# Performance work log

Measured on AMD Instinct MI355X. Metric: run time of the kernel, lower is better.

Reference implementation:

```python
import jax, jax.numpy as jnp
import numpy as np

B, Q, N0, N1, N2 = 2, 16, 4096, 1024, 256
DIM, CTX, HEADS = 296, 288, 8
I1, I2, I3 = 144, 72, 36
EPS = 1e-5  # BatchNorm eps (eval mode)


def setup_inputs():
    key = jax.random.key(0)
    ks = iter(jax.random.split(key, 64))
    def rn(shape, scale=1.0):
        return scale * jax.random.normal(next(ks), shape, dtype=jnp.float32)
    def ru(shape, lo, hi):
        return jax.random.uniform(next(ks), shape, dtype=jnp.float32, minval=lo, maxval=hi)
    def bn(c):  # rows: gamma, beta, running_mean, running_var
        return jnp.stack([1.0 + 0.1 * rn((c,)), 0.1 * rn((c,)), 0.1 * rn((c,)), 1.0 + 0.1 * jnp.abs(rn((c,)))])
    def lin(o, i):
        s = 1.0 / np.sqrt(i)
        return rn((o, i), s), rn((o,), s)
    w1, b1 = lin(DIM, DIM); w2, b2 = lin(I1, DIM)
    a1_w, a1_b = lin(I2, 3); a2_w, a2_b = lin(I1, 128)
    fp1_w1, fp1_b1 = lin(I1, 2 * I1); fp1_w2, fp1_b2 = lin(I2, I1)
    fp2_w1, fp2_b1 = lin(I2, 2 * I2); fp2_w2, fp2_b2 = lin(I3, I2)
    out_w, out_b = lin(1, I3)
    return {
        "x": rn((B, CTX, N2)),
        "bbox_mask": ru((B, Q, HEADS, N2), 0.0, 1.0),
        "sa0_features": rn((B, 3, N0)),
        "sa1_features": rn((B, 128, N1)),
        "sa0_xyz": ru((B, N0, 3), -1.0, 1.0),
        "sa1_xyz": ru((B, N1, 3), -1.0, 1.0),
        "sa2_xyz": ru((B, N2, 3), -1.0, 1.0),
        "w1": w1, "b1": b1, "bn1": bn(DIM),
        "w2": w2, "b2": b2, "bn2": bn(I1),
        "a1_w": a1_w, "a1_b": a1_b,
        "a2_w": a2_w, "a2_b": a2_b,
        "fp1_w1": fp1_w1, "fp1_b1": fp1_b1, "fp1_bn1": bn(I1),
        "fp1_w2": fp1_w2, "fp1_b2": fp1_b2, "fp1_bn2": bn(I2),
        "fp2_w1": fp2_w1, "fp2_b1": fp2_b1, "fp2_bn1": bn(I2),
        "fp2_w2": fp2_w2, "fp2_b2": fp2_b2, "fp2_bn2": bn(I3),
        "out_w": out_w, "out_b": out_b,
    }


def _expand(t, q):
    # tensor.unsqueeze(1).repeat(1, q, 1, 1).flatten(0, 1)
    b = t.shape[0]
    return jnp.broadcast_to(t[:, None], (b, q) + t.shape[1:]).reshape((b * q,) + t.shape[1:])


def _bn(x, p):
    g, b, m, v = p  # (C,) each; x: (BQ, C, N)
    return (x - m[:, None]) * (g * jax.lax.rsqrt(v + EPS))[:, None] + b[:, None]


def _layer(x, W, b, p):
    # SharedMLP layer: 1x1 Conv2d + BN(eval) + ReLU on (BQ, C, N[, 1])
    return jax.nn.relu(_bn(jnp.einsum('oc,bcn->bon', W, x) + b[None, :, None], p))


def _three_interpolate(unknown_xyz, known_xyz, known_feats):
    # three_nn: squared dists (BQ, Nu, Nk) -> 3 smallest; inverse-distance weights
    d2 = jnp.sum((unknown_xyz[:, :, None, :] - known_xyz[:, None, :, :]) ** 2, axis=-1)
    neg_d, idx = jax.lax.top_k(-d2, 3)
    w = 1.0 / (-neg_d + 1e-8)
    w = w / jnp.sum(w, axis=-1, keepdims=True)  # (BQ, Nu, 3)
    g = jax.vmap(lambda f, i: f[:, i])(known_feats, idx)  # (BQ, C, Nu, 3)
    return jnp.sum(g * w[:, None], axis=-1)  # (BQ, C, Nu)


def reference(x, bbox_mask, sa0_features, sa1_features, sa0_xyz, sa1_xyz, sa2_xyz, w1, b1, bn1, w2, b2, bn2, a1_w, a1_b, a2_w, a2_b, fp1_w1, fp1_b1, fp1_bn1, fp1_w2, fp1_b2, fp1_bn2, fp2_w1, fp2_b1, fp2_bn1, fp2_w2, fp2_b2, fp2_bn2, out_w, out_b):
    q = bbox_mask.shape[1]
    h = jnp.concatenate([_expand(x, q), bbox_mask.reshape((-1,) + bbox_mask.shape[2:])], axis=1)  # (BQ, DIM, N2)
    h = _layer(h, w1, b1, bn1)
    h = _layer(h, w2, b2, bn2)  # (BQ, I1, N2)
    f0 = jnp.einsum('oc,bcn->bon', a1_w, sa0_features) + a1_b[None, :, None]  # adapter1
    f1 = jnp.einsum('oc,bcn->bon', a2_w, sa1_features) + a2_b[None, :, None]  # adapter2
    f0, f1 = _expand(f0, q), _expand(f1, q)
    xyz0, xyz1, xyz2 = _expand(sa0_xyz, q), _expand(sa1_xyz, q), _expand(sa2_xyz, q)
    # FP1: propagate sa2 -> sa1, concat [interpolated, skip] as in PointnetFPModule
    h = jnp.concatenate([_three_interpolate(xyz1, xyz2, h), f1], axis=1)
    h = _layer(h, fp1_w1, fp1_b1, fp1_bn1)
    h = _layer(h, fp1_w2, fp1_b2, fp1_bn2)
    # FP2: propagate sa1 -> sa0
    h = jnp.concatenate([_three_interpolate(xyz0, xyz1, h), f0], axis=1)
    h = _layer(h, fp2_w1, fp2_b1, fp2_bn1)
    h = _layer(h, fp2_w2, fp2_b2, fp2_bn2)  # (BQ, I3, N0)
    out = jnp.einsum('oc,bcn->bon', out_w, h) + out_b[None, :, None]  # (BQ, 1, N0)
    return out
```

## Files before the change

### kernel.cpp

```cpp
#include <hip/hip_runtime.h>

#define EPS_BN 1e-5f
typedef float v2f __attribute__((ext_vector_type(2)));

struct LayerDesc {
    const float* W; const float* b; const float* bn;
    float* wt; float* shb; int O; int C;
};
struct HeadArgs {
    LayerDesc l[6];
    const float* a2w; const float* a2b; const float* w3; const float* b3; const float* bn3;
    float* w3c; float* sh3;
    const float* a1w; const float* a1b; const float* w5; const float* b5; const float* bn5;
    float* w5c; float* sh5;
    const float* xyz0; const float* xyz1; const float* xyz2;
    int* idx1; float* wgt1; int* idx2; float* wgt2;
};

__global__ __launch_bounds__(256) void head_kernel(HeadArgs a) {
    const int bx = blockIdx.x, tid = threadIdx.x;
    if (bx < 96) {
        LayerDesc d = a.l[bx / 16];
        int sub = bx % 16;
        int total = d.O * d.C;
        for (int i = sub * 256 + tid; i < total; i += 16 * 256) {
            int c = i / d.O, o = i - (i / d.O) * d.O;
            float sc = 1.f;
            if (d.bn) { float g = d.bn[o], v = d.bn[3 * d.O + o]; sc = g * rsqrtf(v + EPS_BN); }
            d.wt[i] = d.W[(size_t)o * d.C + c] * sc;
        }
        for (int o = sub * 256 + tid; o < d.O; o += 16 * 256) {
            float sc = 1.f, sh = 0.f;
            if (d.bn) {
                float g = d.bn[o], be = d.bn[d.O + o], m = d.bn[2 * d.O + o], v = d.bn[3 * d.O + o];
                sc = g * rsqrtf(v + EPS_BN); sh = be - m * sc;
            }
            d.shb[o] = d.b[o] * sc + sh;
        }
        return;
    } else if (bx < 169) {
        int e = (bx - 96) * 256 + tid;
        if (e < 128 * 144) {
            int k = e / 144, o = e - (e / 144) * 144;
            float sc = a.bn3[o] * rsqrtf(a.bn3[3 * 144 + o] + EPS_BN);
            float s = 0.f;
            for (int c = 0; c < 144; ++c)
                s += a.a2w[c * 128 + k] * a.w3[(size_t)o * 288 + 144 + c];
            a.w3c[k * 144 + o] = s * sc;
        } else if (e < 128 * 144 + 144) {
            int o = e - 128 * 144;
            float g = a.bn3[o], be = a.bn3[144 + o], m = a.bn3[2 * 144 + o], v = a.bn3[3 * 144 + o];
            float sc = g * rsqrtf(v + EPS_BN);
            float s = 0.f;
            for (int c = 0; c < 144; ++c) s += a.w3[(size_t)o * 288 + 144 + c] * a.a2b[c];
            a.sh3[o] = (s + a.b3[o] - m) * sc + be;
        }
        return;
    } else if (bx < 171) {
        int e = (bx - 169) * 256 + tid;
        if (e < 3 * 72) {
            int k = e / 72, o = e - (e / 72) * 72;
            float sc = a.bn5[o] * rsqrtf(a.bn5[3 * 72 + o] + EPS_BN);
            float s = 0.f;
            for (int c = 0; c < 72; ++c)
                s += a.a1w[c * 3 + k] * a.w5[(size_t)o * 144 + 72 + c];
            a.w5c[k * 72 + o] = s * sc;
        } else if (e < 3 * 72 + 72) {
            int o = e - 3 * 72;
            float g = a.bn5[o], be = a.bn5[72 + o], m = a.bn5[2 * 72 + o], v = a.bn5[3 * 72 + o];
            float sc = g * rsqrtf(v + EPS_BN);
            float s = 0.f;
            for (int c = 0; c < 72; ++c) s += a.w5[(size_t)o * 144 + 72 + c] * a.a1b[c];
            a.sh5[o] = (s + a.b5[o] - m) * sc + be;
        }
        return;
    }
    const int NSEG = 8;
    __shared__ float kl[3 * 1024];
    __shared__ float sd[NSEG][32][3];
    __shared__ int   si[NSEG][32][3];
    const float* unknown; const float* known;
    int Nu, Nk, blk, b; int* idx; float* wgt;
    int t = bx - 171;
    if (t < 64) {
        unknown = a.xyz1; known = a.xyz2; Nu = 1024; Nk = 256;
        b = t >> 5; blk = t & 31; idx = a.idx1; wgt = a.wgt1;
    } else {
        t -= 64;
        unknown = a.xyz0; known = a.xyz1; Nu = 4096; Nk = 1024;
        b = t >> 7; blk = t & 127; idx = a.idx2; wgt = a.wgt2;
    }
    for (int i = tid; i < Nk * 3; i += 256) kl[i] = known[(size_t)b * Nk * 3 + i];
    __syncthreads();
    const int u   = tid & 31;
    const int seg = tid >> 5;
    const int n   = blk * 32 + u;
    const float* up = unknown + ((size_t)b * Nu + n) * 3;
    const float ux = up[0], uy = up[1], uz = up[2];
    float d0 = 1e30f, d1 = 1e30f, d2 = 1e30f;
    int i0 = 0, i1 = 0, i2 = 0;
    const int klo = seg * (Nk / NSEG), khi = klo + Nk / NSEG;
    for (int k = klo; k < khi; ++k) {
        float dx = __fsub_rn(ux, kl[3 * k + 0]);
        float dy = __fsub_rn(uy, kl[3 * k + 1]);
        float dz = __fsub_rn(uz, kl[3 * k + 2]);
        float d = __fadd_rn(__fadd_rn(__fmul_rn(dx, dx), __fmul_rn(dy, dy)), __fmul_rn(dz, dz));
        if (d < d0)      { d2 = d1; i2 = i1; d1 = d0; i1 = i0; d0 = d; i0 = k; }
        else if (d < d1) { d2 = d1; i2 = i1; d1 = d;  i1 = k; }
        else if (d < d2) { d2 = d;  i2 = k; }
    }
    sd[seg][u][0] = d0; sd[seg][u][1] = d1; sd[seg][u][2] = d2;
    si[seg][u][0] = i0; si[seg][u][1] = i1; si[seg][u][2] = i2;
    __syncthreads();
    if (tid < 32) {
        float m0 = 1e30f, m1 = 1e30f, m2 = 1e30f;
        int j0 = 0, j1 = 0, j2 = 0;
        for (int s = 0; s < NSEG; ++s)
            for (int c = 0; c < 3; ++c) {
                float d = sd[s][u][c];
                int ii = si[s][u][c];
                if (d < m0)      { m2 = m1; j2 = j1; m1 = m0; j1 = j0; m0 = d; j0 = ii; }
                else if (d < m1) { m2 = m1; j2 = j1; m1 = d;  j1 = ii; }
                else if (d < m2) { m2 = d;  j2 = ii; }
            }
        float w0 = 1.f / (m0 + 1e-8f), w1 = 1.f / (m1 + 1e-8f), w2 = 1.f / (m2 + 1e-8f);
        float s = w0 + w1 + w2;
        size_t base = ((size_t)b * Nu + n) * 3;
        idx[base + 0] = j0; idx[base + 1] = j1; idx[base + 2] = j2;
        wgt[base + 0] = w0 / s; wgt[base + 1] = w1 / s; wgt[base + 2] = w2 / s;
    }
}

template <int BLK, int CT, int O, int OT, bool RELU, int ADD, bool TOUT>
__device__ __forceinline__ void conv_body(
    int nt, int ot, int nb, int tid,
    const float* __restrict__ src0, int qdiv0,
    const float* __restrict__ Wt, const float* __restrict__ shb,
    const float* __restrict__ basep, int qdivb,
    float* __restrict__ outp, int N, float* wlds)
{
    static_assert(OT % 4 == 0, "OT float4 grouping");
    static_assert(CT % 8 == 0 || CT % 8 == 4, "CT pipeline tail");
    const int oBase = ot * OT;
    const int n0 = (nt * BLK + tid) * 4;

    for (int i = tid; i < CT * OT; i += BLK)
        wlds[i] = Wt[(size_t)(i / OT) * O + oBase + (i % OT)];
    __syncthreads();

    const float* s0 = src0 + (size_t)(nb / qdiv0) * CT * N + n0;

    v2f acc[OT][2];
#pragma unroll
    for (int ol = 0; ol < OT; ++ol) { acc[ol][0] = (v2f)0.f; acc[ol][1] = (v2f)0.f; }

    auto loadrow = [&](float (&x)[4], int c) {
        float4 t = *reinterpret_cast<const float4*>(s0 + (size_t)c * N);
        x[0] = t.x; x[1] = t.y; x[2] = t.z; x[3] = t.w;
    };
    auto comprow = [&](const float (&x)[4], int c) {
        v2f x01; x01[0] = x[0]; x01[1] = x[1];
        v2f x23; x23[0] = x[2]; x23[1] = x[3];
#pragma unroll
        for (int g = 0; g < OT / 4; ++g) {
            float4 wv = *reinterpret_cast<const float4*>(&wlds[c * OT + g * 4]);
            float ww[4] = {wv.x, wv.y, wv.z, wv.w};
#pragma unroll
            for (int r = 0; r < 4; ++r) {
                v2f w2; w2[0] = ww[r]; w2[1] = ww[r];
                acc[g * 4 + r][0] = __builtin_elementwise_fma(w2, x01, acc[g * 4 + r][0]);
                acc[g * 4 + r][1] = __builtin_elementwise_fma(w2, x23, acc[g * 4 + r][1]);
            }
        }
    };
    auto loadg = [&](float (&buf)[4][4], int c) {
#pragma unroll
        for (int q = 0; q < 4; ++q) loadrow(buf[q], c + q);
    };
    auto compg = [&](const float (&buf)[4][4], int c) {
#pragma unroll
        for (int q = 0; q < 4; ++q) comprow(buf[q], c + q);
    };

    {
        float xa[4][4], xb[4][4];
        loadg(xa, 0); loadg(xb, 4);
        int c = 0;
#pragma unroll 1
        for (; c + 16 <= CT; c += 8) {
            compg(xa, c);     loadg(xa, c + 8);
            compg(xb, c + 4); loadg(xb, c + 12);
        }
        compg(xa, c);
        if constexpr (CT % 8 == 4) {
            loadg(xa, c + 8);
            compg(xb, c + 4);
            compg(xa, c + 8);
        } else {
            compg(xb, c + 4);
        }
    }

    if constexpr (TOUT) {
#pragma unroll
        for (int j = 0; j < 4; ++j) {
            float4 t;
            t.x = acc[0][j >> 1][j & 1];
            t.y = acc[1][j >> 1][j & 1];
            t.z = acc[2][j >> 1][j & 1];
            t.w = acc[3][j >> 1][j & 1];
            *reinterpret_cast<float4*>(outp + ((size_t)nb * N + n0 + j) * O + oBase) = t;
        }
        return;
    }

    const float* bp = (ADD == 2) ? (basep + ((size_t)(nb / qdivb) * O + oBase) * N + n0) : nullptr;
#pragma unroll
    for (int ol = 0; ol < OT; ++ol) {
        int o = oBase + ol;
        float addv[4];
        if constexpr (ADD == 2) {
            float4 t = *reinterpret_cast<const float4*>(bp + (size_t)ol * N);
            addv[0] = t.x; addv[1] = t.y; addv[2] = t.z; addv[3] = t.w;
        } else if constexpr (ADD == 1) {
            float sb = shb[o];
#pragma unroll
            for (int j = 0; j < 4; ++j) addv[j] = sb;
        } else {
#pragma unroll
            for (int j = 0; j < 4; ++j) addv[j] = 0.f;
        }
        float res[4];
#pragma unroll
        for (int j = 0; j < 4; ++j) {
            float y = acc[ol][j >> 1][j & 1] + addv[j];
            if constexpr (RELU) y = fmaxf(y, 0.f);
            res[j] = y;
        }
        float4 t; t.x = res[0]; t.y = res[1]; t.z = res[2]; t.w = res[3];
        *reinterpret_cast<float4*>(outp + ((size_t)nb * O + o) * N + n0) = t;
    }
}

template <int BLK, int CT, int O, int OT, bool RELU, int ADD, bool TOUT>
__global__ __launch_bounds__(BLK) void conv_swz(
    const float* __restrict__ src0, int qdiv0,
    const float* __restrict__ Wt, const float* __restrict__ shb,
    const float* __restrict__ basep, int qdivb,
    float* __restrict__ outp, int N, int GX, int GY)
{
    __shared__ __align__(16) float wlds[CT * OT];
    int f = blockIdx.x;
    int J = gridDim.x >> 3;
    int j = (f & 7) * J + (f >> 3);
    int ot = j % GY; int r = j / GY;
    int nt = r % GX; int nb = r / GX;
    conv_body<BLK, CT, O, OT, RELU, ADD, TOUT>(
        nt, ot, nb, threadIdx.x, src0, qdiv0, Wt, shb, basep, qdivb, outp, N, wlds);
}

__global__ __launch_bounds__(64) void bases_kernel(
    const float* __restrict__ x, const float* __restrict__ sa1f,
    const float* __restrict__ wt1, const float* __restrict__ sb1,
    const float* __restrict__ w3c, const float* __restrict__ sh3,
    float* __restrict__ base1, float* __restrict__ base3)
{
    __shared__ __align__(16) float wlds[288 * 4];
    const int bx = blockIdx.x, tid = threadIdx.x;
    if (bx < 148) {
        int ot = bx % 74, nb = bx / 74;
        conv_body<64, 288, 296, 4, false, 1, false>(0, ot, nb, tid, x, 1, wt1, sb1, nullptr, 1, base1, 256, wlds);
    } else {
        int lb = bx - 148;
        int nt = lb % 4, ot = (lb / 4) % 36, nb = lb / 144;
        conv_body<64, 128, 144, 4, false, 1, false>(nt, ot, nb, tid, sa1f, 1, w3c, sh3, nullptr, 1, base3, 1024, wlds);
    }
}

__global__ __launch_bounds__(64) void gather_t1_kernel(
    const float* __restrict__ g3t,
    const int* __restrict__ idx, const float* __restrict__ wgt,
    const float* __restrict__ base3,
    float* __restrict__ h3)
{
    int f = blockIdx.x;
    int j = (f & 7) * 64 + (f >> 3);
    int nb = j >> 4, nt = j & 15;
    int lane = threadIdx.x;
    int n = nt * 64 + lane;
    int b = nb >> 4;
    size_t nn = ((size_t)b * 1024 + n) * 3;
    int j0 = idx[nn], j1 = idx[nn + 1], j2 = idx[nn + 2];
    float w0 = wgt[nn], w1 = wgt[nn + 1], w2 = wgt[nn + 2];
    const float* gbase = g3t + (size_t)nb * 256 * 144;
    const float* p0 = gbase + (size_t)j0 * 144;
    const float* p1 = gbase + (size_t)j1 * 144;
    const float* p2 = gbase + (size_t)j2 * 144;
    const float* bb = base3 + (size_t)b * 144 * 1024 + n;
    float* ob = h3 + (size_t)nb * 144 * 1024 + n;
#pragma unroll 1
    for (int cc = 0; cc < 144; cc += 8) {
        float4 a0 = *reinterpret_cast<const float4*>(p0 + cc);
        float4 a0b = *reinterpret_cast<const float4*>(p0 + cc + 4);
        float4 a1 = *reinterpret_cast<const float4*>(p1 + cc);
        float4 a1b = *reinterpret_cast<const float4*>(p1 + cc + 4);
        float4 a2 = *reinterpret_cast<const float4*>(p2 + cc);
        float4 a2b = *reinterpret_cast<const float4*>(p2 + cc + 4);
        float r0[8] = {a0.x, a0.y, a0.z, a0.w, a0b.x, a0b.y, a0b.z, a0b.w};
        float r1[8] = {a1.x, a1.y, a1.z, a1.w, a1b.x, a1b.y, a1b.z, a1b.w};
        float r2[8] = {a2.x, a2.y, a2.z, a2.w, a2b.x, a2b.y, a2b.z, a2b.w};
#pragma unroll
        for (int r = 0; r < 8; ++r) {
            float v = w0 * r0[r] + w1 * r1[r] + w2 * r2[r] + bb[(size_t)(cc + r) * 1024];
            ob[(size_t)(cc + r) * 1024] = fmaxf(v, 0.f);
        }
    }
}

__global__ __launch_bounds__(64) void h6out_kernel(
    const float* __restrict__ g5t,
    const int* __restrict__ idx, const float* __restrict__ wgt,
    const float* __restrict__ sa0,
    const float* __restrict__ w5c, const float* __restrict__ sh5,
    const float* __restrict__ Wt6, const float* __restrict__ shb6,
    const float* __restrict__ wout, const float* __restrict__ bout,
    float* __restrict__ outp)
{
    __shared__ __align__(16) float wlds[72 * 36];
    __shared__ float w5l[3 * 72];
    __shared__ float sh5l[72], ow[36], sh6l[36];
    const int tid = threadIdx.x;
    for (int i = tid; i < 72 * 36; i += 64) wlds[i] = Wt6[i];
    for (int i = tid; i < 216; i += 64) w5l[i] = w5c[i];
    for (int i = tid; i < 72; i += 64) sh5l[i] = sh5[i];
    if (tid < 36) { ow[tid] = wout[tid]; sh6l[tid] = shb6[tid]; }
    __syncthreads();
    int f = blockIdx.x;
    int j = (f & 7) * ((int)gridDim.x >> 3) + (f >> 3);
    const int nb = j >> 6;
    const int nt = j & 63;
    const int n = nt * 64 + tid;
    const int b = nb >> 4;
    size_t nn = ((size_t)b * 4096 + n) * 3;
    const int j0 = idx[nn], j1 = idx[nn + 1], j2 = idx[nn + 2];
    const float w0 = wgt[nn], w1 = wgt[nn + 1], w2 = wgt[nn + 2];
    const float* gbase = g5t + (size_t)nb * 1024 * 72;
    const float* p0 = gbase + (size_t)j0 * 72;
    const float* p1 = gbase + (size_t)j1 * 72;
    const float* p2 = gbase + (size_t)j2 * 72;
    const float* s0 = sa0 + (size_t)b * 3 * 4096 + n;
    const float sx = s0[0], sy = s0[4096], sz = s0[8192];

    v2f acc[18];
#pragma unroll
    for (int o = 0; o < 18; ++o) acc[o] = (v2f)0.f;

    float ra[8][3], rb[8][3];
    auto ld = [&](float (&r)[8][3], int c) {
        float4 a0 = *reinterpret_cast<const float4*>(p0 + c);
        float4 a0b = *reinterpret_cast<const float4*>(p0 + c + 4);
        float4 a1 = *reinterpret_cast<const float4*>(p1 + c);
        float4 a1b = *reinterpret_cast<const float4*>(p1 + c + 4);
        float4 a2 = *reinterpret_cast<const float4*>(p2 + c);
        float4 a2b = *reinterpret_cast<const float4*>(p2 + c + 4);
        r[0][0] = a0.x; r[1][0] = a0.y; r[2][0] = a0.z; r[3][0] = a0.w;
        r[4][0] = a0b.x; r[5][0] = a0b.y; r[6][0] = a0b.z; r[7][0] = a0b.w;
        r[0][1] = a1.x; r[1][1] = a1.y; r[2][1] = a1.z; r[3][1] = a1.w;
        r[4][1] = a1b.x; r[5][1] = a1b.y; r[6][1] = a1b.z; r[7][1] = a1b.w;
        r[0][2] = a2.x; r[1][2] = a2.y; r[2][2] = a2.z; r[3][2] = a2.w;
        r[4][2] = a2b.x; r[5][2] = a2b.y; r[6][2] = a2b.z; r[7][2] = a2b.w;
    };
    auto cp = [&](const float (&r)[8][3], int c) {
#pragma unroll
        for (int q = 0; q < 8; ++q) {
            int cc = c + q;
            float base = w5l[cc] * sx + w5l[72 + cc] * sy + w5l[144 + cc] * sz + sh5l[cc];
            float xv = fmaxf(w0 * r[q][0] + w1 * r[q][1] + w2 * r[q][2] + base, 0.f);
            v2f xv2; xv2[0] = xv; xv2[1] = xv;
#pragma unroll
            for (int g = 0; g < 9; ++g) {
                float4 wv = *reinterpret_cast<const float4*>(&wlds[cc * 36 + g * 4]);
                v2f wa; wa[0] = wv.x; wa[1] = wv.y;
                v2f wb; wb[0] = wv.z; wb[1] = wv.w;
                acc[g * 2 + 0] = __builtin_elementwise_fma(wa, xv2, acc[g * 2 + 0]);
                acc[g * 2 + 1] = __builtin_elementwise_fma(wb, xv2, acc[g * 2 + 1]);
            }
        }
    };
    ld(ra, 0); ld(rb, 8);
    int c = 0;
#pragma unroll 1
    for (; c + 32 <= 72; c += 16) {
        cp(ra, c);     ld(ra, c + 16);
        cp(rb, c + 8); ld(rb, c + 24);
    }
    cp(ra, 48); ld(ra, 64);
    cp(rb, 56);
    cp(ra, 64);

    float r = bout[0];
#pragma unroll
    for (int o = 0; o < 36; ++o) r += ow[o] * fmaxf(acc[o >> 1][o & 1] + sh6l[o], 0.f);
    outp[(size_t)nb * 4096 + n] = r;
}

extern "C" void kernel_launch(void* const* d_in, const int* in_sizes, int n_in,
                              void* d_out, int out_size, void* d_ws, size_t ws_size,
                              hipStream_t stream) {
    const int B = 2, Q = 16, N0 = 4096, N1 = 1024, N2 = 256;
    const int I1 = 144;
    const int NB = B * Q;

    const float* x     = (const float*)d_in[0];
    const float* mask  = (const float*)d_in[1];
    const float* sa0f  = (const float*)d_in[2];
    const float* sa1f  = (const float*)d_in[3];
    const float* xyz0  = (const float*)d_in[4];
    const float* xyz1  = (const float*)d_in[5];
    const float* xyz2  = (const float*)d_in[6];

    float* ws = (float*)d_ws;
    size_t off = 0;
    auto alloc = [&](size_t n) { size_t p = off; off += (n + 15) & ~(size_t)15; return p; };

    size_t wgt1  = alloc((size_t)B * N1 * 3);
    size_t wgt2  = alloc((size_t)B * N0 * 3);
    size_t idx1  = alloc((size_t)B * N1 * 3);
    size_t idx2  = alloc((size_t)B * N0 * 3);
    size_t slotA = alloc((size_t)NB * 296 * N2);
    size_t slotB = alloc((size_t)NB * I1 * N1);
    size_t base1 = alloc((size_t)B * 296 * N2);
    size_t base3 = alloc((size_t)B * I1 * N1);
    size_t wt1 = alloc(296 * 296), sb1 = alloc(296);
    size_t wt2 = alloc(296 * 144), sb2 = alloc(144);
    size_t wt3 = alloc(288 * 144), sb3 = alloc(144);
    size_t wt4 = alloc(144 * 72),  sb4 = alloc(72);
    size_t wt5 = alloc(144 * 72),  sb5 = alloc(72);
    size_t wt6 = alloc(72 * 36),   sb6 = alloc(36);
    size_t w3c = alloc(128 * 144), sh3 = alloc(144);
    size_t w5c = alloc(3 * 72),    sh5 = alloc(72);
    (void)ws_size; (void)in_sizes; (void)n_in;

    auto din = [&](int i) { return (const float*)d_in[i]; };

    HeadArgs ha;
    ha.l[0] = { din(7),  din(8),  din(9),  ws + wt1, ws + sb1, 296, 296 };
    ha.l[1] = { din(10), din(11), din(12), ws + wt2, ws + sb2, 144, 296 };
    ha.l[2] = { din(17), din(18), din(19), ws + wt3, ws + sb3, 144, 288 };
    ha.l[3] = { din(20), din(21), din(22), ws + wt4, ws + sb4, 72, 144 };
    ha.l[4] = { din(23), din(24), din(25), ws + wt5, ws + sb5, 72, 144 };
    ha.l[5] = { din(26), din(27), din(28), ws + wt6, ws + sb6, 36, 72 };
    ha.a2w = din(15); ha.a2b = din(16); ha.w3 = din(17); ha.b3 = din(18); ha.bn3 = din(19);
    ha.w3c = ws + w3c; ha.sh3 = ws + sh3;
    ha.a1w = din(13); ha.a1b = din(14); ha.w5 = din(23); ha.b5 = din(24); ha.bn5 = din(25);
    ha.w5c = ws + w5c; ha.sh5 = ws + sh5;
    ha.xyz0 = xyz0; ha.xyz1 = xyz1; ha.xyz2 = xyz2;
    ha.idx1 = (int*)(ws + idx1); ha.wgt1 = ws + wgt1;
    ha.idx2 = (int*)(ws + idx2); ha.wgt2 = ws + wgt2;
    head_kernel<<<dim3(171 + 64 + 256), 256, 0, stream>>>(ha);

    bases_kernel<<<dim3(436), 64, 0, stream>>>(
        x, sa1f, ws + wt1, ws + sb1, ws + w3c, ws + sh3, ws + base1, ws + base3);

    conv_swz<64, 8, 296, 4, true, 2, false><<<dim3(2368), 64, 0, stream>>>(
        mask, 1, ws + wt1 + 288 * 296, ws + sb1, ws + base1, Q, ws + slotA, N2, 1, 74);

    conv_swz<64, 296, 144, 4, true, 1, false><<<dim3(1152), 64, 0, stream>>>(
        ws + slotA, 1, ws + wt2, ws + sb2, nullptr, 1, ws + slotB, N2, 1, 36);

    conv_swz<64, 144, 144, 4, false, 0, true><<<dim3(1152), 64, 0, stream>>>(
        ws + slotB, 1, ws + wt3, ws + sb3, nullptr, 1, ws + slotA, N2, 1, 36);

    gather_t1_kernel<<<dim3(512), 64, 0, stream>>>(
        ws + slotA, (const int*)(ws + idx1), ws + wgt1, ws + base3, ws + slotB);

    conv_swz<64, 144, 72, 4, true, 1, false><<<dim3(2304), 64, 0, stream>>>(
        ws + slotB, 1, ws + wt4, ws + sb4, nullptr, 1, ws + slotA, N1, 4, 18);

    conv_swz<64, 72, 72, 4, false, 0, true><<<dim3(2304), 64, 0, stream>>>(
        ws + slotA, 1, ws + wt5, ws + sb5, nullptr, 1, ws + slotB, N1, 4, 18);

    h6out_kernel<<<dim3(2048), 64, 0, stream>>>(
        ws + slotB, (const int*)(ws + idx2), ws + wgt2, sa0f,
        ws + w5c, ws + sh5, ws + wt6, ws + sb6, din(29), din(30), (float*)d_out);
}
```

Measured before the change: 174.4 us.

## Split conv reduction across two waves per block and halve gather channel work

The channel (K) loop of the pointwise conv layers is split between two wavefronts in a 128-thread block, and the partial sums are combined through shared memory. This doubles the number of waves in flight for these small-N layers. The gather kernel now splits its 144 channels into two 72-channel halves, using twice as many blocks. The tiny CT=8 mask conv gets a simpler fully unrolled single-wave kernel. The cost is an extra LDS reduction and barrier per block, and only one wave does the epilogue.

```diff
diff --git a/kernel.cpp b/kernel.cpp
--- a/kernel.cpp
+++ b/kernel.cpp
@@ -131,29 +131,11 @@
     }
 }
 
-template <int BLK, int CT, int O, int OT, bool RELU, int ADD, bool TOUT>
-__device__ __forceinline__ void conv_body(
-    int nt, int ot, int nb, int tid,
-    const float* __restrict__ src0, int qdiv0,
-    const float* __restrict__ Wt, const float* __restrict__ shb,
-    const float* __restrict__ basep, int qdivb,
-    float* __restrict__ outp, int N, float* wlds)
-{
-    static_assert(OT % 4 == 0, "OT float4 grouping");
-    static_assert(CT % 8 == 0 || CT % 8 == 4, "CT pipeline tail");
-    const int oBase = ot * OT;
-    const int n0 = (nt * BLK + tid) * 4;
-
-    for (int i = tid; i < CT * OT; i += BLK)
-        wlds[i] = Wt[(size_t)(i / OT) * O + oBase + (i % OT)];
-    __syncthreads();
-
-    const float* s0 = src0 + (size_t)(nb / qdiv0) * CT * N + n0;
-
-    v2f acc[OT][2];
-#pragma unroll
-    for (int ol = 0; ol < OT; ++ol) { acc[ol][0] = (v2f)0.f; acc[ol][1] = (v2f)0.f; }
-
+template <int CTW>
+__device__ __forceinline__ void conv_kloop(
+    const float* __restrict__ s0, int N, const float* wldsw, v2f (&acc)[4][2])
+{
+    static_assert(CTW % 8 == 0 || CTW % 8 == 4, "CT tail");
     auto loadrow = [&](float (&x)[4], int c) {
         float4 t = *reinterpret_cast<const float4*>(s0 + (size_t)c * N);
         x[0] = t.x; x[1] = t.y; x[2] = t.z; x[3] = t.w;
@@ -161,16 +143,13 @@
     auto comprow = [&](const float (&x)[4], int c) {
         v2f x01; x01[0] = x[0]; x01[1] = x[1];
         v2f x23; x23[0] = x[2]; x23[1] = x[3];
-#pragma unroll
-        for (int g = 0; g < OT / 4; ++g) {
-            float4 wv = *reinterpret_cast<const float4*>(&wlds[c * OT + g * 4]);
-            float ww[4] = {wv.x, wv.y, wv.z, wv.w};
-#pragma unroll
-            for (int r = 0; r < 4; ++r) {
-                v2f w2; w2[0] = ww[r]; w2[1] = ww[r];
-                acc[g * 4 + r][0] = __builtin_elementwise_fma(w2, x01, acc[g * 4 + r][0]);
-                acc[g * 4 + r][1] = __builtin_elementwise_fma(w2, x23, acc[g * 4 + r][1]);
-            }
+        float4 wv = *reinterpret_cast<const float4*>(wldsw + c * 4);
+        float ww[4] = {wv.x, wv.y, wv.z, wv.w};
+#pragma unroll
+        for (int r = 0; r < 4; ++r) {
+            v2f w2; w2[0] = ww[r]; w2[1] = ww[r];
+            acc[r][0] = __builtin_elementwise_fma(w2, x01, acc[r][0]);
+            acc[r][1] = __builtin_elementwise_fma(w2, x23, acc[r][1]);
         }
     };
     auto loadg = [&](float (&buf)[4][4], int c) {
@@ -181,25 +160,61 @@
 #pragma unroll
         for (int q = 0; q < 4; ++q) comprow(buf[q], c + q);
     };
-
-    {
-        float xa[4][4], xb[4][4];
-        loadg(xa, 0); loadg(xb, 4);
-        int c = 0;
+    float xa[4][4], xb[4][4];
+    loadg(xa, 0); loadg(xb, 4);
+    int c = 0;
 #pragma unroll 1
-        for (; c + 16 <= CT; c += 8) {
-            compg(xa, c);     loadg(xa, c + 8);
-            compg(xb, c + 4); loadg(xb, c + 12);
-        }
-        compg(xa, c);
-        if constexpr (CT % 8 == 4) {
-            loadg(xa, c + 8);
-            compg(xb, c + 4);
-            compg(xa, c + 8);
-        } else {
-            compg(xb, c + 4);
-        }
-    }
+    for (; c + 16 <= CTW; c += 8) {
+        compg(xa, c);     loadg(xa, c + 8);
+        compg(xb, c + 4); loadg(xb, c + 12);
+    }
+    compg(xa, c);
+    if constexpr (CTW % 8 == 4) {
+        loadg(xa, c + 8);
+        compg(xb, c + 4);
+        compg(xa, c + 8);
+    } else {
+        compg(xb, c + 4);
+    }
+}
+
+template <int CT0, int CT1, int O, bool RELU, int ADD, bool TOUT>
+__device__ __forceinline__ void conv2w(
+    int nt, int ot, int nb, int tid,
+    const float* __restrict__ src0, int qdiv0,
+    const float* __restrict__ Wt, const float* __restrict__ shb,
+    const float* __restrict__ basep, int qdivb,
+    float* __restrict__ outp, int N, float* wlds, float* sred)
+{
+    constexpr int CTALL = CT0 + CT1;
+    const int wid = tid >> 6, lane = tid & 63;
+    const int oBase = ot * 4;
+    const int n0 = (nt * 64 + lane) * 4;
+
+    for (int i = tid; i < CTALL * 4; i += 128)
+        wlds[i] = Wt[(size_t)(i >> 2) * O + oBase + (i & 3)];
+    __syncthreads();
+
+    const int c0 = wid ? CT0 : 0;
+    const float* s0 = src0 + (size_t)(nb / qdiv0) * CTALL * N + (size_t)c0 * N + n0;
+
+    v2f acc[4][2];
+#pragma unroll
+    for (int r = 0; r < 4; ++r) { acc[r][0] = (v2f)0.f; acc[r][1] = (v2f)0.f; }
+
+    if (wid == 0) conv_kloop<CT0>(s0, N, wlds, acc);
+    else          conv_kloop<CT1>(s0, N, wlds + CT0 * 4, acc);
+
+    if (wid == 1) {
+#pragma unroll
+        for (int i = 0; i < 16; ++i)
+            sred[i * 64 + lane] = acc[i >> 2][(i >> 1) & 1][i & 1];
+    }
+    __syncthreads();
+    if (wid != 0) return;
+#pragma unroll
+    for (int i = 0; i < 16; ++i)
+        acc[i >> 2][(i >> 1) & 1][i & 1] += sred[i * 64 + lane];
 
     if constexpr (TOUT) {
 #pragma unroll
@@ -213,7 +228,92 @@
         }
         return;
     }
-
+    const float* bp = (ADD == 2) ? (basep + ((size_t)(nb / qdivb) * O + oBase) * N + n0) : nullptr;
+#pragma unroll
+    for (int ol = 0; ol < 4; ++ol) {
+        int o = oBase + ol;
+        float addv[4];
+        if constexpr (ADD == 2) {
+            float4 t = *reinterpret_cast<const float4*>(bp + (size_t)ol * N);
+            addv[0] = t.x; addv[1] = t.y; addv[2] = t.z; addv[3] = t.w;
+        } else if constexpr (ADD == 1) {
+            float sb = shb[o];
+#pragma unroll
+            for (int j = 0; j < 4; ++j) addv[j] = sb;
+        } else {
+#pragma unroll
+            for (int j = 0; j < 4; ++j) addv[j] = 0.f;
+        }
+        float res[4];
+#pragma unroll
+        for (int j = 0; j < 4; ++j) {
+            float y = acc[ol][j >> 1][j & 1] + addv[j];
+            if constexpr (RELU) y = fmaxf(y, 0.f);
+            res[j] = y;
+        }
+        float4 t; t.x = res[0]; t.y = res[1]; t.z = res[2]; t.w = res[3];
+        *reinterpret_cast<float4*>(outp + ((size_t)nb * O + o) * N + n0) = t;
+    }
+}
+
+template <int CT0, int CT1, int O, bool RELU, int ADD, bool TOUT>
+__global__ __launch_bounds__(128) void conv_ks2(
+    const float* __restrict__ src0, int qdiv0,
+    const float* __restrict__ Wt, const float* __restrict__ shb,
+    const float* __restrict__ basep, int qdivb,
+    float* __restrict__ outp, int N, int GX, int GY)
+{
+    __shared__ __align__(16) float wlds[(CT0 + CT1) * 4];
+    __shared__ float sred[16 * 64];
+    int f = blockIdx.x;
+    int J = gridDim.x >> 3;
+    int j = (f & 7) * J + (f >> 3);
+    int ot = j % GY; int r = j / GY;
+    int nt = r % GX; int nb = r / GX;
+    conv2w<CT0, CT1, O, RELU, ADD, TOUT>(
+        nt, ot, nb, threadIdx.x, src0, qdiv0, Wt, shb, basep, qdivb, outp, N, wlds, sred);
+}
+
+template <int CT, int O, int OT, bool RELU, int ADD>
+__global__ __launch_bounds__(64) void conv_swz(
+    const float* __restrict__ src0, int qdiv0,
+    const float* __restrict__ Wt, const float* __restrict__ shb,
+    const float* __restrict__ basep, int qdivb,
+    float* __restrict__ outp, int N, int GX, int GY)
+{
+    __shared__ __align__(16) float wlds[CT * OT];
+    int f = blockIdx.x;
+    int J = gridDim.x >> 3;
+    int j = (f & 7) * J + (f >> 3);
+    int ot = j % GY; int r = j / GY;
+    int nt = r % GX; int nb = r / GX;
+    const int lane = threadIdx.x;
+    const int oBase = ot * OT;
+    const int n0 = (nt * 64 + lane) * 4;
+    for (int i = lane; i < CT * OT; i += 64)
+        wlds[i] = Wt[(size_t)(i / OT) * O + oBase + (i % OT)];
+    __builtin_amdgcn_wave_barrier();
+    const float* s0 = src0 + (size_t)(nb / qdiv0) * CT * N + n0;
+    v2f acc[OT][2];
+#pragma unroll
+    for (int ol = 0; ol < OT; ++ol) { acc[ol][0] = (v2f)0.f; acc[ol][1] = (v2f)0.f; }
+#pragma unroll
+    for (int c = 0; c < CT; ++c) {
+        float4 t = *reinterpret_cast<const float4*>(s0 + (size_t)c * N);
+        v2f x01; x01[0] = t.x; x01[1] = t.y;
+        v2f x23; x23[0] = t.z; x23[1] = t.w;
+#pragma unroll
+        for (int g = 0; g < OT / 4; ++g) {
+            float4 wv = *reinterpret_cast<const float4*>(&wlds[c * OT + g * 4]);
+            float ww[4] = {wv.x, wv.y, wv.z, wv.w};
+#pragma unroll
+            for (int r = 0; r < 4; ++r) {
+                v2f w2; w2[0] = ww[r]; w2[1] = ww[r];
+                acc[g * 4 + r][0] = __builtin_elementwise_fma(w2, x01, acc[g * 4 + r][0]);
+                acc[g * 4 + r][1] = __builtin_elementwise_fma(w2, x23, acc[g * 4 + r][1]);
+            }
+        }
+    }
     const float* bp = (ADD == 2) ? (basep + ((size_t)(nb / qdivb) * O + oBase) * N + n0) : nullptr;
 #pragma unroll
     for (int ol = 0; ol < OT; ++ol) {
@@ -242,38 +342,22 @@
     }
 }
 
-template <int BLK, int CT, int O, int OT, bool RELU, int ADD, bool TOUT>
-__global__ __launch_bounds__(BLK) void conv_swz(
-    const float* __restrict__ src0, int qdiv0,
-    const float* __restrict__ Wt, const float* __restrict__ shb,
-    const float* __restrict__ basep, int qdivb,
-    float* __restrict__ outp, int N, int GX, int GY)
-{
-    __shared__ __align__(16) float wlds[CT * OT];
-    int f = blockIdx.x;
-    int J = gridDim.x >> 3;
-    int j = (f & 7) * J + (f >> 3);
-    int ot = j % GY; int r = j / GY;
-    int nt = r % GX; int nb = r / GX;
-    conv_body<BLK, CT, O, OT, RELU, ADD, TOUT>(
-        nt, ot, nb, threadIdx.x, src0, qdiv0, Wt, shb, basep, qdivb, outp, N, wlds);
-}
-
-__global__ __launch_bounds__(64) void bases_kernel(
+__global__ __launch_bounds__(128) void bases_kernel(
     const float* __restrict__ x, const float* __restrict__ sa1f,
     const float* __restrict__ wt1, const float* __restrict__ sb1,
     const float* __restrict__ w3c, const float* __restrict__ sh3,
     float* __restrict__ base1, float* __restrict__ base3)
 {
     __shared__ __align__(16) float wlds[288 * 4];
+    __shared__ float sred[16 * 64];
     const int bx = blockIdx.x, tid = threadIdx.x;
     if (bx < 148) {
         int ot = bx % 74, nb = bx / 74;
-        conv_body<64, 288, 296, 4, false, 1, false>(0, ot, nb, tid, x, 1, wt1, sb1, nullptr, 1, base1, 256, wlds);
+        conv2w<144, 144, 296, false, 1, false>(0, ot, nb, tid, x, 1, wt1, sb1, nullptr, 1, base1, 256, wlds, sred);
     } else {
         int lb = bx - 148;
         int nt = lb % 4, ot = (lb / 4) % 36, nb = lb / 144;
-        conv_body<64, 128, 144, 4, false, 1, false>(nt, ot, nb, tid, sa1f, 1, w3c, sh3, nullptr, 1, base3, 1024, wlds);
+        conv2w<64, 64, 144, false, 1, false>(nt, ot, nb, tid, sa1f, 1, w3c, sh3, nullptr, 1, base3, 1024, wlds, sred);
     }
 }
 
@@ -284,8 +368,9 @@
     float* __restrict__ h3)
 {
     int f = blockIdx.x;
-    int j = (f & 7) * 64 + (f >> 3);
-    int nb = j >> 4, nt = j & 15;
+    int j = (f & 7) * 128 + (f >> 3);
+    int cseg = j & 1; int rest = j >> 1;
+    int nb = rest >> 4, nt = rest & 15;
     int lane = threadIdx.x;
     int n = nt * 64 + lane;
     int b = nb >> 4;
@@ -298,8 +383,9 @@
     const float* p2 = gbase + (size_t)j2 * 144;
     const float* bb = base3 + (size_t)b * 144 * 1024 + n;
     float* ob = h3 + (size_t)nb * 144 * 1024 + n;
+    const int cs = cseg * 72;
 #pragma unroll 1
-    for (int cc = 0; cc < 144; cc += 8) {
+    for (int cc = cs; cc < cs + 72; cc += 8) {
         float4 a0 = *reinterpret_cast<const float4*>(p0 + cc);
         float4 a0b = *reinterpret_cast<const float4*>(p0 + cc + 4);
         float4 a1 = *reinterpret_cast<const float4*>(p1 + cc);
@@ -459,25 +545,25 @@
     ha.idx2 = (int*)(ws + idx2); ha.wgt2 = ws + wgt2;
     head_kernel<<<dim3(171 + 64 + 256), 256, 0, stream>>>(ha);
 
-    bases_kernel<<<dim3(436), 64, 0, stream>>>(
+    bases_kernel<<<dim3(436), 128, 0, stream>>>(
         x, sa1f, ws + wt1, ws + sb1, ws + w3c, ws + sh3, ws + base1, ws + base3);
 
-    conv_swz<64, 8, 296, 4, true, 2, false><<<dim3(2368), 64, 0, stream>>>(
+    conv_swz<8, 296, 4, true, 2><<<dim3(2368), 64, 0, stream>>>(
         mask, 1, ws + wt1 + 288 * 296, ws + sb1, ws + base1, Q, ws + slotA, N2, 1, 74);
 
-    conv_swz<64, 296, 144, 4, true, 1, false><<<dim3(1152), 64, 0, stream>>>(
+    conv_ks2<152, 144, 144, true, 1, false><<<dim3(1152), 128, 0, stream>>>(
         ws + slotA, 1, ws + wt2, ws + sb2, nullptr, 1, ws + slotB, N2, 1, 36);
 
-    conv_swz<64, 144, 144, 4, false, 0, true><<<dim3(1152), 64, 0, stream>>>(
+    conv_ks2<72, 72, 144, false, 0, true><<<dim3(1152), 128, 0, stream>>>(
         ws + slotB, 1, ws + wt3, ws + sb3, nullptr, 1, ws + slotA, N2, 1, 36);
 
-    gather_t1_kernel<<<dim3(512), 64, 0, stream>>>(
+    gather_t1_kernel<<<dim3(1024), 64, 0, stream>>>(
         ws + slotA, (const int*)(ws + idx1), ws + wgt1, ws + base3, ws + slotB);
 
-    conv_swz<64, 144, 72, 4, true, 1, false><<<dim3(2304), 64, 0, stream>>>(
+    conv_ks2<72, 72, 72, true, 1, false><<<dim3(2304), 128, 0, stream>>>(
         ws + slotB, 1, ws + wt4, ws + sb4, nullptr, 1, ws + slotA, N1, 4, 18);
 
-    conv_swz<64, 72, 72, 4, false, 0, true><<<dim3(2304), 64, 0, stream>>>(
+    conv_ks2<36, 36, 72, false, 0, true><<<dim3(2304), 128, 0, stream>>>(
         ws + slotA, 1, ws + wt5, ws + sb5, nullptr, 1, ws + slotB, N1, 4, 18);
 
     h6out_kernel<<<dim3(2048), 64, 0, stream>>>(
```

Result: faster. 162.5 us (-6.9%).
